# Optimization experiments

Hardware: AMD Instinct MI355X
Metric: run time of the kernel (lower is better)

The kernel has to match this reference:

```python
import jax, jax.numpy as jnp
import numpy as np
import math

D_MODEL = 2048
N_HEADS = 16
D_K = D_MODEL // N_HEADS


def setup_inputs() -> dict:
    key = jax.random.key(0)
    k0, k1, k2, k3, k4 = jax.random.split(key, 5)
    B, T = 2, 2048
    x = jax.random.normal(k0, (B, T, D_MODEL), dtype=jnp.float32)
    s = 1.0 / math.sqrt(D_MODEL)
    W_qkv = jax.random.normal(k1, (3 * D_MODEL, D_MODEL), dtype=jnp.float32) * s
    b_qkv = jax.random.normal(k2, (3 * D_MODEL,), dtype=jnp.float32) * 0.01
    W_out = jax.random.normal(k3, (D_MODEL, D_MODEL), dtype=jnp.float32) * s
    b_out = jax.random.normal(k4, (D_MODEL,), dtype=jnp.float32) * 0.01
    return {"x": x, "W_qkv": W_qkv, "b_qkv": b_qkv, "W_out": W_out, "b_out": b_out}


def reference(x, W_qkv, b_qkv, W_out, b_out):
    B, T, C = x.shape
    qkv = x @ W_qkv.T + b_qkv                      # [B,T,3C]
    q, k, v = jnp.split(qkv, 3, axis=-1)
    # [B,T,C] -> [B,H,T,Dk]
    def to_heads(t):
        return t.reshape(B, T, N_HEADS, D_K).transpose(0, 2, 1, 3)
    q, k, v = to_heads(q), to_heads(k), to_heads(v)
    scale = 1.0 / math.sqrt(D_K)
    scores = jnp.einsum('bhqd,bhkd->bhqk', q, k) * scale   # [B,H,T,T]
    causal = jnp.tril(jnp.ones((T, T), dtype=bool))
    neg = jnp.finfo(scores.dtype).min
    scores = jnp.where(causal[None, None], scores, neg)
    attn = jax.nn.softmax(scores, axis=-1)
    out = jnp.einsum('bhqk,bhkd->bhqd', attn, v)           # [B,H,T,Dk]
    out = out.transpose(0, 2, 1, 3).reshape(B, T, C)
    return out @ W_out.T + b_out
```

## Files before the change

kernel.cpp:

```cpp
#include <hip/hip_runtime.h>
#include <stdint.h>

typedef short bf16x8 __attribute__((ext_vector_type(8)));
typedef float f32x4 __attribute__((ext_vector_type(4)));
typedef float f32x16 __attribute__((ext_vector_type(16)));
typedef unsigned short u16;
typedef unsigned int u32;

__device__ __forceinline__ u16 f2bf(float f) {
    u32 x = __float_as_uint(f);
    x += 0x7fffu + ((x >> 16) & 1u);
    return (u16)(x >> 16);
}
__device__ __forceinline__ u32 pack_bf2(float a, float b) {
    return (u32)f2bf(a) | ((u32)f2bf(b) << 16);
}

union Frag4 { u32 u[4]; bf16x8 v; };

__device__ __forceinline__ void gload16(const u16* g, u16* l) {
    __builtin_amdgcn_global_load_lds(
        (__attribute__((address_space(1))) void*)g,
        (__attribute__((address_space(3))) void*)l,
        16, 0, 0);
}

__global__ void cvt_f32_bf16(const float* __restrict__ in, u16* __restrict__ out, long n8) {
    long stride = (long)gridDim.x * blockDim.x;
    for (long i = (long)blockIdx.x * blockDim.x + threadIdx.x; i < n8; i += stride) {
        const float4* p = (const float4*)(in + i * 8);
        float4 a = p[0], b = p[1];
        uint4 o;
        o.x = pack_bf2(a.x, a.y);
        o.y = pack_bf2(a.z, a.w);
        o.z = pack_bf2(b.x, b.y);
        o.w = pack_bf2(b.z, b.w);
        ((uint4*)out)[i] = o;
    }
}

template<int OBF>
__global__ __launch_bounds__(256, 2) void gemm_nt(
    const u16* __restrict__ A, const u16* __restrict__ B,
    const float* __restrict__ bias, void* __restrict__ out,
    int K, int ldo, int gxsh)
{
    __shared__ __align__(16) u16 lA[2 * 128 * 64];
    __shared__ __align__(16) u16 lB[2 * 128 * 64];
    const int tid  = threadIdx.x;
    const int lane = tid & 63;
    const int w    = tid >> 6;
    const int wm = (w >> 1) * 64, wn = (w & 1) * 64;

    const int nwg = gridDim.x;
    const int bid = blockIdx.x;
    const int swz = (bid & 7) * (nwg >> 3) + (bid >> 3);
    const int bm = (swz & ((1 << gxsh) - 1)) * 128;
    const int bn = (swz >> gxsh) * 128;

    const int lr = lane >> 3;
    const u32 sb = (u32)((lane & 7) * 16);
    const int NT = K >> 6;

    auto stage = [&](int bb, int k0) {
#pragma unroll
        for (int i = 0; i < 4; ++i) {
            const int c = w * 4 + i;
            const int row = c * 8 + lr;
            const u32 col = (sb ^ ((u32)(row & 7) << 4)) >> 1;
            gload16(A + (size_t)(bm + row) * K + k0 + col, lA + bb * 8192 + c * 512);
            gload16(B + (size_t)(bn + row) * K + k0 + col, lB + bb * 8192 + c * 512);
        }
    };

    f32x4 acc[4][4];
#pragma unroll
    for (int i = 0; i < 4; ++i)
#pragma unroll
        for (int j = 0; j < 4; ++j)
#pragma unroll
            for (int r = 0; r < 4; ++r) acc[i][j][r] = 0.f;

    stage(0, 0);
    stage(1, 64);
    asm volatile("s_waitcnt vmcnt(8)" ::: "memory");
    __builtin_amdgcn_sched_barrier(0);
    __builtin_amdgcn_s_barrier();
    __builtin_amdgcn_sched_barrier(0);

    for (int t = 0; t < NT; ++t) {
        const int cur = t & 1;
        const char* pA = (const char*)(lA + cur * 8192);
        const char* pB = (const char*)(lB + cur * 8192);
#pragma unroll
        for (int kk = 0; kk < 2; ++kk) {
            bf16x8 af[4], bfr[4];
#pragma unroll
            for (int f = 0; f < 4; ++f) {
                const int m = wm + f * 16 + (lane & 15);
                const u32 byt = (u32)(kk * 64 + (lane >> 4) * 16) ^ ((u32)(m & 7) << 4);
                af[f]  = *(const bf16x8*)(pA + m * 128 + byt);
                const int n = wn + f * 16 + (lane & 15);
                const u32 bytb = (u32)(kk * 64 + (lane >> 4) * 16) ^ ((u32)(n & 7) << 4);
                bfr[f] = *(const bf16x8*)(pB + n * 128 + bytb);
            }
            __builtin_amdgcn_s_setprio(1);
#pragma unroll
            for (int i = 0; i < 4; ++i)
#pragma unroll
                for (int j = 0; j < 4; ++j)
                    acc[i][j] = __builtin_amdgcn_mfma_f32_16x16x32_bf16(af[i], bfr[j], acc[i][j], 0, 0, 0);
            __builtin_amdgcn_s_setprio(0);
        }
        __builtin_amdgcn_sched_barrier(0);
        __builtin_amdgcn_s_barrier();
        __builtin_amdgcn_sched_barrier(0);
        if (t + 2 < NT) {
            stage(cur, (t + 2) * 64);
            asm volatile("s_waitcnt vmcnt(8)" ::: "memory");
        } else {
            asm volatile("s_waitcnt vmcnt(0)" ::: "memory");
        }
        __builtin_amdgcn_sched_barrier(0);
        __builtin_amdgcn_s_barrier();
        __builtin_amdgcn_sched_barrier(0);
    }

#pragma unroll
    for (int i = 0; i < 4; ++i) {
        int m0 = bm + wm + i * 16 + ((lane >> 4) << 2);
#pragma unroll
        for (int j = 0; j < 4; ++j) {
            int n = bn + wn + j * 16 + (lane & 15);
            float bv = bias[n];
#pragma unroll
            for (int r = 0; r < 4; ++r) {
                float v = acc[i][j][r] + bv;
                if constexpr (OBF != 0)
                    ((u16*)out)[(size_t)(m0 + r) * ldo + n] = f2bf(v);
                else
                    ((float*)out)[(size_t)(m0 + r) * ldo + n] = v;
            }
        }
    }
}

__global__ __launch_bounds__(256) void transpose_v(
    const u16* __restrict__ qkv, u16* __restrict__ vt)
{
    __shared__ u16 lt[64 * 64];
    const int tid = threadIdx.x;
    const int bid = blockIdx.x;
    const int tt    = bid & 31;
    const int dtile = (bid >> 5) & 1;
    const int h     = (bid >> 6) & 15;
    const int b     = bid >> 10;
    const u16* src = qkv + ((size_t)b * 2048 + tt * 64) * 6144 + 4096 + h * 128 + dtile * 64;

    const int r = tid >> 2, ce = (tid & 3) * 16;
    uint4 a0 = *(const uint4*)(src + (size_t)r * 6144 + ce);
    uint4 a1 = *(const uint4*)(src + (size_t)r * 6144 + ce + 8);
    const u32 swz = (u32)((r & 7) << 4);
    *(uint4*)((char*)lt + r * 128 + (((u32)(ce * 2)) ^ swz)) = a0;
    *(uint4*)((char*)lt + r * 128 + (((u32)(ce * 2 + 16)) ^ swz)) = a1;
    __syncthreads();

    const int d = tid >> 2;
    u16* dst = vt + ((size_t)(b * 16 + h) * 128 + dtile * 64 + d) * 2048 + tt * 64;
#pragma unroll
    for (int it = 0; it < 2; ++it) {
        const int t0 = (tid & 3) * 8 + it * 32;
        union { u16 hh[8]; uint4 q4; } u;
#pragma unroll
        for (int uu = 0; uu < 8; ++uu) {
            int trow = t0 + uu;
            u32 byt = (u32)(trow * 128) + (((u32)(d * 2)) ^ ((u32)((trow & 7) << 4)));
            u.hh[uu] = *(const u16*)((const char*)lt + byt);
        }
        *(uint4*)(dst + t0) = u.q4;
    }
}

__constant__ unsigned char QT_TAB[24] = {15,15,7,14,14,13,13,6,12,12,11,11,5,10,10,9,9,4,8,8,3,2,1,0};
__constant__ unsigned char CK_TAB[24] = {0,1,2,0,1,0,1,2,0,1,0,1,2,0,1,0,1,2,0,1,2,2,2,2};

__global__ __launch_bounds__(256) void attn_fwd(
    const u16* __restrict__ qkv, const u16* __restrict__ vt,
    u16* __restrict__ obuf, float* __restrict__ pout, float* __restrict__ pml)
{
    __shared__ __align__(16) u16 lK[2 * 32 * 128];
    __shared__ __align__(16) u16 lV[2 * 128 * 32];
    const int tid  = threadIdx.x;
    const int lane = tid & 63;
    const int w    = tid >> 6;
    const int g    = lane >> 5;
    const int ql   = lane & 31;

    const int bid  = blockIdx.x;
    const int item = bid >> 5;
    const int bh   = bid & 31;
    const int qt   = QT_TAB[item];
    const int ck   = CK_TAB[item];
    const int b = bh >> 4, h = bh & 15;
    const size_t rowbase = (size_t)b * 2048;
    const int qb = qt * 128;
    const int qw = qb + w * 32;
    const int q  = qw + ql;
    const int t_lo = (ck == 1) ? (2 * qt + 2) : 0;
    const int t_hi = (ck == 0) ? (2 * qt + 2) : (4 * qt + 4);

    const u16* Khead = qkv + rowbase * 6144 + 2048 + h * 128;
    const u16* Vth   = vt + (size_t)bh * 128 * 2048;

    bf16x8 qf[8];
    {
        const u16* qrow = qkv + (rowbase + q) * 6144 + h * 128;
#pragma unroll
        for (int ch = 0; ch < 8; ++ch)
            qf[ch] = *(const bf16x8*)(qrow + ch * 16 + g * 8);
    }

    f32x16 acc[4];
#pragma unroll
    for (int dt = 0; dt < 4; ++dt)
#pragma unroll
        for (int r = 0; r < 16; ++r) acc[dt][r] = 0.f;

    float m_run = -1e30f, l_run = 0.f;
    const float C2 = 0.08838834764831845f * 1.44269504088896341f;

    auto stage = [&](int bb, int t) {
        const int kb = t * 32;
#pragma unroll
        for (int i = 0; i < 2; ++i) {
            const int c = w * 2 + i;
            const int kr = c * 4 + (lane >> 4);
            const u32 kcol = (((u32)((lane & 15) * 16)) ^ ((u32)(kr & 7) << 4)) >> 1;
            gload16(Khead + (size_t)(kb + kr) * 6144 + kcol,
                    lK + bb * 4096 + c * 512);
            const int vr = c * 16 + (lane >> 2);
            const u32 vcol = (((u32)((lane & 3) * 16)) ^ ((u32)(vr & 3) << 4)) >> 1;
            gload16(Vth + (size_t)vr * 2048 + kb + vcol,
                    lV + bb * 4096 + c * 512);
        }
    };

    stage(0, t_lo);
    __syncthreads();
    int buf = 0;

    for (int t = t_lo; t < t_hi; ++t) {
        const int kb = t * 32;
        if (t + 1 < t_hi) stage(buf ^ 1, t + 1);

        if (kb <= qw + 31) {
            const char* lKb = (const char*)(lK + buf * 4096);
            const char* lVb = (const char*)(lV + buf * 4096);
            const bool diag = (kb == qw);

            bf16x8 kf[8];
            const u32 ksw = ((u32)ql & 7) << 4;
#pragma unroll
            for (int ch = 0; ch < 8; ++ch)
                kf[ch] = *(const bf16x8*)(lKb + ql * 256 + (((u32)(ch * 32 + g * 16)) ^ ksw));

            f32x16 s_;
#pragma unroll
            for (int r = 0; r < 16; ++r) s_[r] = 0.f;
            __builtin_amdgcn_s_setprio(1);
#pragma unroll
            for (int ch = 0; ch < 8; ++ch)
                s_ = __builtin_amdgcn_mfma_f32_32x32x16_bf16(kf[ch], qf[ch], s_, 0, 0, 0);
            __builtin_amdgcn_s_setprio(0);

            float p[16];
            float tmax = -1e30f;
#pragma unroll
            for (int r = 0; r < 16; ++r) {
                int crow = (r & 3) + 8 * (r >> 2) + 4 * g;
                float v = s_[r];
                if (diag && (crow > ql)) v = -1e30f;
                p[r] = v;
                tmax = fmaxf(tmax, v);
            }
            tmax = fmaxf(tmax, __shfl_xor(tmax, 32));
            if (!__all(tmax <= m_run + 8.0f)) {
                float mnew  = fmaxf(m_run, tmax);
                float alpha = exp2f((m_run - mnew) * C2);
#pragma unroll
                for (int dt = 0; dt < 4; ++dt) acc[dt] = acc[dt] * alpha;
                l_run *= alpha;
                m_run = mnew;
            }
            float ssum = 0.f;
#pragma unroll
            for (int r = 0; r < 16; ++r) {
                float e = exp2f((p[r] - m_run) * C2);
                p[r] = e;
                ssum += e;
            }
            ssum += __shfl_xor(ssum, 32);
            l_run += ssum;

            u32 wb[8], sw[8];
#pragma unroll
            for (int j = 0; j < 8; ++j) wb[j] = pack_bf2(p[2 * j], p[2 * j + 1]);
#pragma unroll
            for (int j = 0; j < 8; ++j) sw[j] = __shfl_xor(wb[j], 32);
            Frag4 pf0, pf1;
#pragma unroll
            for (int u = 0; u < 4; ++u) {
                const bool own = (g == (u >> 1));
                pf0.u[u] = own ? wb[2 * g + (u & 1)]     : sw[2 * g + (u & 1)];
                pf1.u[u] = own ? wb[4 + 2 * g + (u & 1)] : sw[4 + 2 * g + (u & 1)];
            }

            __builtin_amdgcn_s_setprio(1);
#pragma unroll
            for (int dt = 0; dt < 4; ++dt) {
                const u32 vrow = (u32)(dt * 32 + ql);
                const u32 vsw = (vrow & 3) << 4;
                bf16x8 v0 = *(const bf16x8*)(lVb + vrow * 64 + (((u32)(g * 16)) ^ vsw));
                bf16x8 v1 = *(const bf16x8*)(lVb + vrow * 64 + (((u32)(32 + g * 16)) ^ vsw));
                acc[dt] = __builtin_amdgcn_mfma_f32_32x32x16_bf16(v0, pf0.v, acc[dt], 0, 0, 0);
                acc[dt] = __builtin_amdgcn_mfma_f32_32x32x16_bf16(v1, pf1.v, acc[dt], 0, 0, 0);
            }
            __builtin_amdgcn_s_setprio(0);
        }
        __syncthreads();
        buf ^= 1;
    }

    if (ck == 2) {
        const float inv_l = 1.0f / l_run;
        u16* orow = obuf + (rowbase + q) * 2048 + h * 128;
#pragma unroll
        for (int dt = 0; dt < 4; ++dt) {
#pragma unroll
            for (int rr = 0; rr < 4; ++rr) {
                int d0 = dt * 32 + rr * 8 + g * 4;
                int r0 = rr * 4;
                u32 w0 = pack_bf2(acc[dt][r0] * inv_l,     acc[dt][r0 + 1] * inv_l);
                u32 w1 = pack_bf2(acc[dt][r0 + 2] * inv_l, acc[dt][r0 + 3] * inv_l);
                *(u32*)(orow + d0)     = w0;
                *(u32*)(orow + d0 + 2) = w1;
            }
        }
    } else {
        const int slot = (((bh << 3) | (qt - 8)) << 1) + ck;
        const int qloc = w * 32 + ql;
        float* po = pout + (size_t)slot * 16384 + (size_t)qloc * 128;
#pragma unroll
        for (int dt = 0; dt < 4; ++dt) {
#pragma unroll
            for (int rr = 0; rr < 4; ++rr) {
                int d0 = dt * 32 + rr * 8 + g * 4;
                int r0 = rr * 4;
                float4 v4 = make_float4(acc[dt][r0], acc[dt][r0 + 1],
                                        acc[dt][r0 + 2], acc[dt][r0 + 3]);
                *(float4*)(po + d0) = v4;
            }
        }
        if (g == 0) {
            float2* pm = (float2*)pml + slot * 128 + qloc;
            *pm = make_float2(m_run, l_run);
        }
    }
}

__global__ __launch_bounds__(256) void attn_merge(
    const float* __restrict__ pout, const float* __restrict__ pml,
    u16* __restrict__ obuf)
{
    const int bid = blockIdx.x;
    const int bh = bid >> 3, qto = bid & 7;
    const int b = bh >> 4, h = bh & 15;
    const int tid = threadIdx.x;
    const int qloc = tid >> 1, half = (tid & 1) * 64;
    const int base = ((bh << 3) | qto) << 1;
    const float C2 = 0.08838834764831845f * 1.44269504088896341f;

    const float2 ml0 = ((const float2*)pml)[(base + 0) * 128 + qloc];
    const float2 ml1 = ((const float2*)pml)[(base + 1) * 128 + qloc];
    const float ms = fmaxf(ml0.x, ml1.x);
    const float w0 = exp2f((ml0.x - ms) * C2);
    const float w1 = exp2f((ml1.x - ms) * C2);
    const float inv = 1.0f / (ml0.y * w0 + ml1.y * w1);

    const float* p0 = pout + (size_t)(base + 0) * 16384 + (size_t)qloc * 128 + half;
    const float* p1 = pout + (size_t)(base + 1) * 16384 + (size_t)qloc * 128 + half;
    const int qrow = (8 + qto) * 128 + qloc;
    u16* orow = obuf + ((size_t)b * 2048 + qrow) * 2048 + h * 128 + half;
#pragma unroll
    for (int j = 0; j < 64; j += 4) {
        float4 a = *(const float4*)(p0 + j);
        float4 c = *(const float4*)(p1 + j);
        float o0 = (a.x * w0 + c.x * w1) * inv;
        float o1 = (a.y * w0 + c.y * w1) * inv;
        float o2 = (a.z * w0 + c.z * w1) * inv;
        float o3 = (a.w * w0 + c.w * w1) * inv;
        *(u32*)(orow + j)     = pack_bf2(o0, o1);
        *(u32*)(orow + j + 2) = pack_bf2(o2, o3);
    }
}

extern "C" void kernel_launch(void* const* d_in, const int* in_sizes, int n_in,
                              void* d_out, int out_size, void* d_ws, size_t ws_size,
                              hipStream_t stream) {
    (void)in_sizes; (void)n_in; (void)out_size; (void)ws_size;
    const float* x    = (const float*)d_in[0];
    const float* Wqkv = (const float*)d_in[1];
    const float* bqkv = (const float*)d_in[2];
    const float* Wout = (const float*)d_in[3];
    const float* bout = (const float*)d_in[4];

    char* ws = (char*)d_ws;
    u16* xb  = (u16*)ws;
    u16* wqb = (u16*)(ws + (size_t)16777216);
    u16* qkv = (u16*)(ws + (size_t)41943040);
    u16* ob  = xb;
    u16* vtb = wqb;
    u16* wob = wqb;
    float* pml = (float*)(ws + (size_t)33554432);
    float* pO  = (float*)d_out;

    cvt_f32_bf16<<<2048, 256, 0, stream>>>(x, xb, 8388608L / 8);
    cvt_f32_bf16<<<2048, 256, 0, stream>>>(Wqkv, wqb, 12582912L / 8);
    gemm_nt<1><<<1536, 256, 0, stream>>>(xb, wqb, bqkv, qkv, 2048, 6144, 5);
    transpose_v<<<2048, 256, 0, stream>>>(qkv, vtb);
    attn_fwd<<<768, 256, 0, stream>>>(qkv, vtb, ob, pO, pml);
    attn_merge<<<256, 256, 0, stream>>>(pO, pml, ob);
    cvt_f32_bf16<<<2048, 256, 0, stream>>>(Wout, wob, 4194304L / 8);
    gemm_nt<0><<<512, 256, 0, stream>>>(ob, wob, bout, d_out, 2048, 2048, 5);
}
```

Baseline: 312.9 us.

## Rebalance causal attention split-K across more work items and store partials in bf16

After: 308.1 us. Within noise of the previous version (-1.5%).

```diff
diff --git a/kernel.cpp b/kernel.cpp
--- a/kernel.cpp
+++ b/kernel.cpp
@@ -14,6 +14,9 @@
 }
 __device__ __forceinline__ u32 pack_bf2(float a, float b) {
     return (u32)f2bf(a) | ((u32)f2bf(b) << 16);
+}
+__device__ __forceinline__ float bf2f(u16 v) {
+    return __uint_as_float(((u32)v) << 16);
 }
 
 union Frag4 { u32 u[4]; bf16x8 v; };
@@ -181,12 +184,14 @@
     }
 }
 
-__constant__ unsigned char QT_TAB[24] = {15,15,7,14,14,13,13,6,12,12,11,11,5,10,10,9,9,4,8,8,3,2,1,0};
-__constant__ unsigned char CK_TAB[24] = {0,1,2,0,1,0,1,2,0,1,0,1,2,0,1,0,1,2,0,1,2,2,2,2};
+__constant__ unsigned char QT_TAB[30] = {11,11, 5,15,15,15,10,10,14,14,14, 9, 9, 4,13,13,13,12,12,12, 8, 8, 7, 7, 3, 6, 6, 2, 1, 0};
+__constant__ unsigned char TLO_TAB[30]= { 0,24, 0, 0,22,43, 0,22, 0,20,40, 0,20, 0, 0,19,38, 0,18,36, 0,18, 0,16, 0, 0,14, 0, 0, 0};
+__constant__ unsigned char THI_TAB[30]= {24,48,24,22,43,64,22,44,20,40,60,20,40,20,19,38,56,18,36,52,18,36,16,32,16,14,28,12, 8, 4};
+__constant__ unsigned char SL_TAB[30] = {10,11,255,21,22,23, 8, 9,18,19,20, 6, 7,255,15,16,17,12,13,14, 4, 5, 2, 3,255, 0, 1,255,255,255};
 
 __global__ __launch_bounds__(256) void attn_fwd(
     const u16* __restrict__ qkv, const u16* __restrict__ vt,
-    u16* __restrict__ obuf, float* __restrict__ pout, float* __restrict__ pml)
+    u16* __restrict__ obuf, u16* __restrict__ pout, float* __restrict__ pml)
 {
     __shared__ __align__(16) u16 lK[2 * 32 * 128];
     __shared__ __align__(16) u16 lV[2 * 128 * 32];
@@ -200,14 +205,14 @@
     const int item = bid >> 5;
     const int bh   = bid & 31;
     const int qt   = QT_TAB[item];
-    const int ck   = CK_TAB[item];
+    const int slot = SL_TAB[item];
+    const int t_lo = TLO_TAB[item];
+    const int t_hi = THI_TAB[item];
     const int b = bh >> 4, h = bh & 15;
     const size_t rowbase = (size_t)b * 2048;
     const int qb = qt * 128;
     const int qw = qb + w * 32;
     const int q  = qw + ql;
-    const int t_lo = (ck == 1) ? (2 * qt + 2) : 0;
-    const int t_hi = (ck == 0) ? (2 * qt + 2) : (4 * qt + 4);
 
     const u16* Khead = qkv + rowbase * 6144 + 2048 + h * 128;
     const u16* Vth   = vt + (size_t)bh * 128 * 2048;
@@ -331,7 +336,7 @@
         buf ^= 1;
     }
 
-    if (ck == 2) {
+    if (slot == 255) {
         const float inv_l = 1.0f / l_run;
         u16* orow = obuf + (rowbase + q) * 2048 + h * 128;
 #pragma unroll
@@ -347,60 +352,82 @@
             }
         }
     } else {
-        const int slot = (((bh << 3) | (qt - 8)) << 1) + ck;
+        const int sg = bh * 24 + slot;
         const int qloc = w * 32 + ql;
-        float* po = pout + (size_t)slot * 16384 + (size_t)qloc * 128;
+        u16* po = pout + (size_t)sg * 16384 + (size_t)qloc * 128;
 #pragma unroll
         for (int dt = 0; dt < 4; ++dt) {
 #pragma unroll
             for (int rr = 0; rr < 4; ++rr) {
                 int d0 = dt * 32 + rr * 8 + g * 4;
                 int r0 = rr * 4;
-                float4 v4 = make_float4(acc[dt][r0], acc[dt][r0 + 1],
-                                        acc[dt][r0 + 2], acc[dt][r0 + 3]);
-                *(float4*)(po + d0) = v4;
+                u32 w0 = pack_bf2(acc[dt][r0],     acc[dt][r0 + 1]);
+                u32 w1 = pack_bf2(acc[dt][r0 + 2], acc[dt][r0 + 3]);
+                *(u32*)(po + d0)     = w0;
+                *(u32*)(po + d0 + 2) = w1;
             }
         }
         if (g == 0) {
-            float2* pm = (float2*)pml + slot * 128 + qloc;
+            float2* pm = (float2*)pml + sg * 128 + qloc;
             *pm = make_float2(m_run, l_run);
         }
     }
 }
 
 __global__ __launch_bounds__(256) void attn_merge(
-    const float* __restrict__ pout, const float* __restrict__ pml,
+    const u16* __restrict__ pout, const float* __restrict__ pml,
     u16* __restrict__ obuf)
 {
     const int bid = blockIdx.x;
-    const int bh = bid >> 3, qto = bid & 7;
+    const int bh = bid & 31, j = bid >> 5;
+    const int qt = 6 + j;
     const int b = bh >> 4, h = bh & 15;
     const int tid = threadIdx.x;
     const int qloc = tid >> 1, half = (tid & 1) * 64;
-    const int base = ((bh << 3) | qto) << 1;
+    const int f  = (qt < 12) ? 2 : 3;
+    const int sb = (qt < 12) ? (qt - 6) * 2 : 12 + (qt - 12) * 3;
+    const int base = bh * 24 + sb;
     const float C2 = 0.08838834764831845f * 1.44269504088896341f;
 
-    const float2 ml0 = ((const float2*)pml)[(base + 0) * 128 + qloc];
-    const float2 ml1 = ((const float2*)pml)[(base + 1) * 128 + qloc];
-    const float ms = fmaxf(ml0.x, ml1.x);
-    const float w0 = exp2f((ml0.x - ms) * C2);
-    const float w1 = exp2f((ml1.x - ms) * C2);
-    const float inv = 1.0f / (ml0.y * w0 + ml1.y * w1);
-
-    const float* p0 = pout + (size_t)(base + 0) * 16384 + (size_t)qloc * 128 + half;
-    const float* p1 = pout + (size_t)(base + 1) * 16384 + (size_t)qloc * 128 + half;
-    const int qrow = (8 + qto) * 128 + qloc;
+    float mv[3], lv[3], wv[3];
+    float ms = -1e30f;
+#pragma unroll
+    for (int i = 0; i < 3; ++i) {
+        if (i < f) {
+            float2 ml = ((const float2*)pml)[(base + i) * 128 + qloc];
+            mv[i] = ml.x; lv[i] = ml.y;
+            ms = fmaxf(ms, ml.x);
+        }
+    }
+    float L = 0.f;
+#pragma unroll
+    for (int i = 0; i < 3; ++i) {
+        if (i < f) {
+            wv[i] = exp2f((mv[i] - ms) * C2);
+            L += lv[i] * wv[i];
+        }
+    }
+    const float inv = 1.0f / L;
+
+    const int qrow = qt * 128 + qloc;
     u16* orow = obuf + ((size_t)b * 2048 + qrow) * 2048 + h * 128 + half;
 #pragma unroll
-    for (int j = 0; j < 64; j += 4) {
-        float4 a = *(const float4*)(p0 + j);
-        float4 c = *(const float4*)(p1 + j);
-        float o0 = (a.x * w0 + c.x * w1) * inv;
-        float o1 = (a.y * w0 + c.y * w1) * inv;
-        float o2 = (a.z * w0 + c.z * w1) * inv;
-        float o3 = (a.w * w0 + c.w * w1) * inv;
-        *(u32*)(orow + j)     = pack_bf2(o0, o1);
-        *(u32*)(orow + j + 2) = pack_bf2(o2, o3);
+    for (int j0 = 0; j0 < 64; j0 += 8) {
+        float o[8];
+#pragma unroll
+        for (int e = 0; e < 8; ++e) o[e] = 0.f;
+#pragma unroll
+        for (int i = 0; i < 3; ++i) {
+            if (i < f) {
+                bf16x8 v = *(const bf16x8*)(pout + (size_t)(base + i) * 16384
+                                            + (size_t)qloc * 128 + half + j0);
+#pragma unroll
+                for (int e = 0; e < 8; ++e) o[e] += wv[i] * bf2f((u16)v[e]);
+            }
+        }
+#pragma unroll
+        for (int e = 0; e < 8; e += 2)
+            *(u32*)(orow + j0 + e) = pack_bf2(o[e] * inv, o[e + 1] * inv);
     }
 }
 
@@ -422,14 +449,14 @@
     u16* vtb = wqb;
     u16* wob = wqb;
     float* pml = (float*)(ws + (size_t)33554432);
-    float* pO  = (float*)d_out;
+    u16* pO  = (u16*)d_out;
 
     cvt_f32_bf16<<<2048, 256, 0, stream>>>(x, xb, 8388608L / 8);
     cvt_f32_bf16<<<2048, 256, 0, stream>>>(Wqkv, wqb, 12582912L / 8);
     gemm_nt<1><<<1536, 256, 0, stream>>>(xb, wqb, bqkv, qkv, 2048, 6144, 5);
     transpose_v<<<2048, 256, 0, stream>>>(qkv, vtb);
-    attn_fwd<<<768, 256, 0, stream>>>(qkv, vtb, ob, pO, pml);
-    attn_merge<<<256, 256, 0, stream>>>(pO, pml, ob);
+    attn_fwd<<<960, 256, 0, stream>>>(qkv, vtb, ob, pO, pml);
+    attn_merge<<<320, 256, 0, stream>>>(pO, pml, ob);
     cvt_f32_bf16<<<2048, 256, 0, stream>>>(Wout, wob, 4194304L / 8);
     gemm_nt<0><<<512, 256, 0, stream>>>(ob, wob, bout, d_out, 2048, 2048, 5);
 }
```
